# Kernel tuning notes

Measured on AMD Instinct MI355X. Metric: run time of the kernel, lower is better.

Reference implementation:

```python
import jax, jax.numpy as jnp
import numpy as np

EMBED_DIM = 1024
N_HEADS = 16
HEAD_DIM = EMBED_DIM // N_HEADS


def setup_inputs() -> dict:
    key = jax.random.key(0)
    k_x, k_wi, k_bi, k_wo, k_bo = jax.random.split(key, 5)
    B, N, C = 4, 2048, EMBED_DIM
    scale = 1.0 / np.sqrt(C)
    return {
        "x": jax.random.normal(k_x, (B, N, C), dtype=jnp.float32),
        "w_in": jax.random.normal(k_wi, (C, 3 * C), dtype=jnp.float32) * scale,
        "b_in": jax.random.normal(k_bi, (3 * C,), dtype=jnp.float32) * 0.01,
        "w_out": jax.random.normal(k_wo, (C, C), dtype=jnp.float32) * scale,
        "b_out": jax.random.normal(k_bo, (C,), dtype=jnp.float32) * 0.01,
    }


def reference(x, w_in, b_in, w_out, b_out):
    B, N, C = x.shape
    H, D = N_HEADS, HEAD_DIM
    qkv = x @ w_in + b_in  # (B, N, 3C)
    q, k, v = jnp.split(qkv, 3, axis=-1)
    # (B, H, N, D)
    q = q.reshape(B, N, H, D).transpose(0, 2, 1, 3)
    k = k.reshape(B, N, H, D).transpose(0, 2, 1, 3)
    v = v.reshape(B, N, H, D).transpose(0, 2, 1, 3)
    # Naive attention: full (B,H,N,N) scores, NO sqrt(d) scaling (as in source)
    scores = jnp.einsum("bhnd,bhmd->bhnm", q, k)
    attn = jax.nn.softmax(scores, axis=-1)
    out = jnp.einsum("bhnm,bhmd->bhnd", attn, v)
    out = out.transpose(0, 2, 1, 3).reshape(B, N, C)
    return out @ w_out + b_out
```

## Files before the change

### kernel.cpp

```cpp
#include <hip/hip_runtime.h>
#include <hip/hip_bf16.h>
#include <stdint.h>

typedef __attribute__((ext_vector_type(8))) __bf16 bf8v;
typedef __attribute__((ext_vector_type(4))) float f4v;

#define L2E 1.44269504088896f

__device__ __forceinline__ unsigned short f2bf(float f) {
  union { float f; unsigned u; } v; v.f = f;
  unsigned r = v.u + 0x7fffu + ((v.u >> 16) & 1u);
  return (unsigned short)(r >> 16);
}

__device__ __forceinline__ unsigned pk2bf(float f0, float f1) {
  union { __hip_bfloat162 h; unsigned u; } c;
  c.h = __float22bfloat162_rn(make_float2(f0, f1));
  return c.u;
}

__device__ __forceinline__ float exp2_hw(float x) {
  return __builtin_amdgcn_exp2f(x);
}

__device__ __forceinline__ void gl_lds16(const void* g, void* l) {
  __builtin_amdgcn_global_load_lds(
      (__attribute__((address_space(1))) void*)(g),
      (__attribute__((address_space(3))) void*)(l), 16, 0, 0);
}

__global__ void prep_kernel(const float* __restrict__ x,
                            const float* __restrict__ w_in,
                            const float* __restrict__ w_out,
                            unsigned short* __restrict__ xb,
                            unsigned short* __restrict__ wiT,
                            unsigned short* __restrict__ woT) {
  __shared__ float tile[32][33];
  int bx = blockIdx.x;
  if (bx < 8192) {
    int i = bx * 256 + threadIdx.x;
    float4 v = ((const float4*)x)[i];
    ushort4 o;
    o.x = f2bf(v.x); o.y = f2bf(v.y); o.z = f2bf(v.z); o.w = f2bf(v.w);
    ((ushort4*)xb)[i] = o;
    return;
  }
  int idx = bx - 8192;
  int bxx = idx & 127, byy = idx >> 7;
  const float* in; unsigned short* out; int C, c0;
  if (bxx < 96) { in = w_in;  out = wiT; C = 3072; c0 = bxx * 32; }
  else          { in = w_out; out = woT; C = 1024; c0 = (bxx - 96) * 32; }
  int r0 = byy * 32;
  int tx = threadIdx.x & 31, ty = threadIdx.x >> 5;
#pragma unroll
  for (int j = 0; j < 4; ++j)
    tile[ty + 8 * j][tx] = in[(size_t)(r0 + ty + 8 * j) * C + c0 + tx];
  __syncthreads();
#pragma unroll
  for (int j = 0; j < 4; ++j)
    out[(size_t)(c0 + ty + 8 * j) * 1024 + r0 + tx] = f2bf(tile[tx][ty + 8 * j]);
}

template <int MODE>
__global__ __launch_bounds__(512, 2) void gemm256(
    const unsigned short* __restrict__ A,
    const unsigned short* __restrict__ BT,
    const float* __restrict__ bias,
    void* __restrict__ Cv,
    unsigned short* __restrict__ vtg,
    int N, int K, int nbx, float scale) {
  __shared__ __align__(16) unsigned short As[2][256 * 64];
  __shared__ __align__(16) unsigned short Bs[2][128 * 64];
  const int tid = threadIdx.x;
  const int wave = tid >> 6, lane = tid & 63;
  const int lo = lane & 15, hi = lane >> 4;
  const int wm = wave >> 1, wn = wave & 1;

  const int cpx = gridDim.x >> 3;
  const int s = (blockIdx.x & 7) * cpx + (blockIdx.x >> 3);
  const int by = s / nbx, bx = s - by * nbx;
  const int m0 = by * 256, n0 = bx * 128;

  const int srow = lane >> 3;
  const int scol = (((lane & 7) ^ (srow & 7)) * 8);
  const unsigned short* gA = A + (size_t)(m0 + wave * 8 + srow) * K + scol;
  const unsigned short* gB = BT + (size_t)(n0 + wave * 8 + srow) * K + scol;

  const int csw0 = ((hi ^ (lo & 7)) * 8);
  const int csw1 = (((4 + hi) ^ (lo & 7)) * 8);
  const int rA = wm * 64;
  const int rB = wn * 64;

  f4v acc[4][4] = {};
  const int nt = K >> 6;

#pragma unroll
  for (int j = 0; j < 4; ++j)
    gl_lds16(gA + (size_t)(j * 64) * K, &As[0][(j * 64 + wave * 8) * 64]);
#pragma unroll
  for (int j = 0; j < 2; ++j)
    gl_lds16(gB + (size_t)(j * 64) * K, &Bs[0][(j * 64 + wave * 8) * 64]);

  for (int t = 0; t < nt; ++t) {
    const int c = t & 1;
    __builtin_amdgcn_s_barrier();
    __builtin_amdgcn_sched_barrier(0);
    if (t + 1 < nt) {
      const unsigned short* gA1 = gA + (size_t)(t + 1) * 64;
      const unsigned short* gB1 = gB + (size_t)(t + 1) * 64;
#pragma unroll
      for (int j = 0; j < 4; ++j)
        gl_lds16(gA1 + (size_t)(j * 64) * K, &As[c ^ 1][(j * 64 + wave * 8) * 64]);
#pragma unroll
      for (int j = 0; j < 2; ++j)
        gl_lds16(gB1 + (size_t)(j * 64) * K, &Bs[c ^ 1][(j * 64 + wave * 8) * 64]);
      asm volatile("s_waitcnt vmcnt(6)" ::: "memory");
    } else {
      asm volatile("s_waitcnt vmcnt(0)" ::: "memory");
    }
    __builtin_amdgcn_sched_barrier(0);
    __builtin_amdgcn_s_barrier();
    __builtin_amdgcn_sched_barrier(0);

    bf8v b[4][2];
#pragma unroll
    for (int fn = 0; fn < 4; ++fn) {
      b[fn][0] = *(const bf8v*)&Bs[c][(rB + fn * 16 + lo) * 64 + csw0];
      b[fn][1] = *(const bf8v*)&Bs[c][(rB + fn * 16 + lo) * 64 + csw1];
    }
#pragma unroll
    for (int p = 0; p < 2; ++p) {
      bf8v a[2][2];
#pragma unroll
      for (int i = 0; i < 2; ++i) {
        a[i][0] = *(const bf8v*)&As[c][(rA + (p * 2 + i) * 16 + lo) * 64 + csw0];
        a[i][1] = *(const bf8v*)&As[c][(rA + (p * 2 + i) * 16 + lo) * 64 + csw1];
      }
      __builtin_amdgcn_s_setprio(1);
#pragma unroll
      for (int ks = 0; ks < 2; ++ks)
#pragma unroll
        for (int i = 0; i < 2; ++i)
#pragma unroll
          for (int fn = 0; fn < 4; ++fn)
            acc[p * 2 + i][fn] = __builtin_amdgcn_mfma_f32_16x16x32_bf16(
                a[i][ks], b[fn][ks], acc[p * 2 + i][fn], 0, 0, 0);
      __builtin_amdgcn_s_setprio(0);
    }
  }

#pragma unroll
  for (int i = 0; i < 4; ++i) {
#pragma unroll
    for (int j = 0; j < 4; ++j) {
      const int col = n0 + wn * 64 + j * 16 + lo;
      const int row0 = m0 + wm * 64 + i * 16 + hi * 4;
      if (MODE == 0) {
        float* C = (float*)Cv;
#pragma unroll
        for (int r = 0; r < 4; ++r)
          C[(size_t)(row0 + r) * N + col] = acc[i][j][r] + bias[col];
      } else {
        unsigned short* C = (unsigned short*)Cv;
        const float bb = bias[col];
        if (col < 2048) {
          const float sc = (col < 1024) ? scale : 1.0f;
#pragma unroll
          for (int r = 0; r < 4; ++r)
            C[(size_t)(row0 + r) * 2048 + col] = f2bf((acc[i][j][r] + bb) * sc);
        } else {
          const int d = (col - 2048) & 63, hh = (col - 2048) >> 6;
          const int bbt = row0 >> 11, tok = row0 & 2047;
          ushort4 o;
          o.x = f2bf(acc[i][j][0] + bb);
          o.y = f2bf(acc[i][j][1] + bb);
          o.z = f2bf(acc[i][j][2] + bb);
          o.w = f2bf(acc[i][j][3] + bb);
          *(ushort4*)&vtg[((((size_t)bbt * 16 + hh) * 64 + d) * 2048) + tok] = o;
        }
      }
    }
  }
}

#define FSTR 72

__global__ __launch_bounds__(256, 2) void flash_attn(
    const unsigned short* __restrict__ qk,
    const unsigned short* __restrict__ vtg,
    unsigned short* __restrict__ y) {
  __shared__ __align__(16) unsigned short Ps[256 * FSTR];
  __shared__ __align__(16) unsigned short Kt[2][64 * FSTR];
  __shared__ __align__(16) unsigned short Vt[2][64 * FSTR];
  const int tid = threadIdx.x;
  const int wave = tid >> 6, lane = tid & 63;
  const int lo = lane & 15, hi = lane >> 4;

  const int lin = blockIdx.x;
  const int swz = (lin & 7) * 64 + (lin >> 3);
  const int q0 = (swz & 7) << 8;
  const int h  = (swz >> 3) & 15;
  const int b  = swz >> 7;

  const size_t base = (size_t)b * 2048 * 2048;
  const int qoff = h * 64, koff = 1024 + h * 64;
  const unsigned short* vsrc = vtg + (size_t)(b * 16 + h) * 64 * 2048;

  const int m_st = tid >> 3, c_st = tid & 7;
  const unsigned short* kg = qk + base + koff;
  float4 rk0, rk1, rv0, rv1;
  auto kv_load = [&](int kt) {
    const int mb = kt * 64;
    rk0 = *(const float4*)(kg + (size_t)(mb + m_st) * 2048 + c_st * 8);
    rk1 = *(const float4*)(kg + (size_t)(mb + m_st + 32) * 2048 + c_st * 8);
    rv0 = *(const float4*)(vsrc + (size_t)m_st * 2048 + mb + c_st * 8);
    rv1 = *(const float4*)(vsrc + (size_t)(m_st + 32) * 2048 + mb + c_st * 8);
  };
  auto kv_write = [&](int buf) {
    *(float4*)&Kt[buf][m_st * FSTR + c_st * 8] = rk0;
    *(float4*)&Kt[buf][(m_st + 32) * FSTR + c_st * 8] = rk1;
    *(float4*)&Vt[buf][m_st * FSTR + c_st * 8] = rv0;
    *(float4*)&Vt[buf][(m_st + 32) * FSTR + c_st * 8] = rv1;
  };

  kv_load(0);

#pragma unroll
  for (int i = 0; i < 8; ++i) {
    int cid = i * 256 + tid;
    int m = cid >> 3, c = cid & 7;
    *(float4*)&Ps[m * FSTR + c * 8] =
        *(const float4*)(qk + base + (size_t)(q0 + m) * 2048 + qoff + c * 8);
  }
  __syncthreads();
  bf8v bq[4][2];
#pragma unroll
  for (int qt = 0; qt < 4; ++qt)
#pragma unroll
    for (int ks = 0; ks < 2; ++ks)
      bq[qt][ks] = *(const bf8v*)&Ps[(wave * 64 + qt * 16 + lo) * FSTR + ks * 32 + hi * 8];

  f4v O[4][4] = {};
  f4v acc_l[4] = {};
  union { bf8v v; unsigned short u[8]; } onesu;
#pragma unroll
  for (int i = 0; i < 8; ++i) onesu.u[i] = 0x3F80;
  const bf8v ones = onesu.v;

  kv_write(0);
  kv_load(1);
  asm volatile("s_waitcnt lgkmcnt(0)" ::: "memory");
  __builtin_amdgcn_s_barrier();
  asm volatile("" ::: "memory");

  for (int kt = 0; kt < 32; ++kt) {
    const int c = kt & 1;
    if (kt < 31) {
      kv_write(c ^ 1);
      if (kt < 30) kv_load(kt + 2);
    }

#pragma unroll
    for (int ct = 0; ct < 4; ++ct) {
      f4v s[4] = {{}, {}, {}, {}};
      __builtin_amdgcn_s_setprio(1);
#pragma unroll
      for (int ks = 0; ks < 2; ++ks) {
        bf8v ak = *(const bf8v*)&Kt[c][(ct * 16 + lo) * FSTR + ks * 32 + hi * 8];
#pragma unroll
        for (int qt = 0; qt < 4; ++qt)
          s[qt] = __builtin_amdgcn_mfma_f32_16x16x32_bf16(ak, bq[qt][ks], s[qt], 0, 0, 0);
      }
      __builtin_amdgcn_s_setprio(0);
#pragma unroll
      for (int qt = 0; qt < 4; ++qt) {
        float p0 = exp2_hw(s[qt][0]), p1 = exp2_hw(s[qt][1]);
        float p2 = exp2_hw(s[qt][2]), p3 = exp2_hw(s[qt][3]);
        uint2 w; w.x = pk2bf(p0, p1); w.y = pk2bf(p2, p3);
        *(uint2*)&Ps[(wave * 64 + qt * 16 + lo) * FSTR + ct * 16 + hi * 4] = w;
      }
    }

#pragma unroll
    for (int ks = 0; ks < 2; ++ks) {
      bf8v ap[4];
#pragma unroll
      for (int qt = 0; qt < 4; ++qt)
        ap[qt] = *(const bf8v*)&Ps[(wave * 64 + qt * 16 + lo) * FSTR + ks * 32 + hi * 8];
      __builtin_amdgcn_s_setprio(1);
#pragma unroll
      for (int qt = 0; qt < 4; ++qt)
        acc_l[qt] = __builtin_amdgcn_mfma_f32_16x16x32_bf16(ap[qt], ones, acc_l[qt], 0, 0, 0);
#pragma unroll
      for (int dt = 0; dt < 4; ++dt) {
        bf8v bv = *(const bf8v*)&Vt[c][(dt * 16 + lo) * FSTR + ks * 32 + hi * 8];
#pragma unroll
        for (int qt = 0; qt < 4; ++qt)
          O[qt][dt] = __builtin_amdgcn_mfma_f32_16x16x32_bf16(ap[qt], bv, O[qt][dt], 0, 0, 0);
      }
      __builtin_amdgcn_s_setprio(0);
    }

    asm volatile("s_waitcnt lgkmcnt(0)" ::: "memory");
    __builtin_amdgcn_s_barrier();
    asm volatile("" ::: "memory");
  }

#pragma unroll
  for (int qt = 0; qt < 4; ++qt) {
#pragma unroll
    for (int r = 0; r < 4; ++r) {
      float inv = 1.f / acc_l[qt][r];
      int row = q0 + wave * 64 + qt * 16 + hi * 4 + r;
      size_t orow = ((size_t)b * 2048 + row) * 1024 + h * 64;
#pragma unroll
      for (int dt = 0; dt < 4; ++dt)
        y[orow + dt * 16 + lo] = f2bf(O[qt][dt][r] * inv);
    }
  }
}

extern "C" void kernel_launch(void* const* d_in, const int* in_sizes, int n_in,
                              void* d_out, int out_size, void* d_ws, size_t ws_size,
                              hipStream_t stream) {
  (void)in_sizes; (void)n_in; (void)out_size; (void)ws_size;
  const float* x     = (const float*)d_in[0];
  const float* w_in  = (const float*)d_in[1];
  const float* b_in  = (const float*)d_in[2];
  const float* w_out = (const float*)d_in[3];
  const float* b_out = (const float*)d_in[4];

  unsigned short* xb  = (unsigned short*)d_ws;
  unsigned short* wiT = xb  + (size_t)8192 * 1024;
  unsigned short* woT = wiT + (size_t)3072 * 1024;
  unsigned short* qk  = woT + (size_t)1024 * 1024;
  unsigned short* vtg = qk  + (size_t)8192 * 2048;
  unsigned short* yb  = vtg + (size_t)64 * 64 * 2048;

  prep_kernel<<<12288, 256, 0, stream>>>(x, w_in, w_out, xb, wiT, woT);

  gemm256<1><<<768, 512, 0, stream>>>(xb, wiT, b_in, qk, vtg, 3072, 1024, 24, L2E);
  flash_attn<<<512, 256, 0, stream>>>(qk, vtg, yb);
  gemm256<0><<<256, 512, 0, stream>>>(yb, woT, b_out, d_out, nullptr, 1024, 1024, 8, 1.0f);
}
```

Measured before the change: 274.8 us.

## Use 256x256 tiles with eight-phase pipelined staging for QKV projection GEMM

```diff
diff --git a/kernel.cpp b/kernel.cpp
--- a/kernel.cpp
+++ b/kernel.cpp
@@ -61,14 +61,133 @@
     out[(size_t)(c0 + ty + 8 * j) * 1024 + r0 + tx] = f2bf(tile[tx][ty + 8 * j]);
 }
 
-template <int MODE>
-__global__ __launch_bounds__(512, 2) void gemm256(
+__global__ __launch_bounds__(512, 2) void gemm1_8ph(
     const unsigned short* __restrict__ A,
     const unsigned short* __restrict__ BT,
     const float* __restrict__ bias,
-    void* __restrict__ Cv,
+    unsigned short* __restrict__ qk,
     unsigned short* __restrict__ vtg,
-    int N, int K, int nbx, float scale) {
+    int K, int nbx, float scale) {
+  __shared__ __align__(16) unsigned short As[2][256 * 64];
+  __shared__ __align__(16) unsigned short Bs[2][256 * 64];
+  const int tid = threadIdx.x;
+  const int wave = tid >> 6, lane = tid & 63;
+  const int lo = lane & 15, hi = lane >> 4;
+  const int wm = wave >> 2, wn = wave & 3;
+
+  const int cpx = gridDim.x >> 3;
+  const int s = (blockIdx.x & 7) * cpx + (blockIdx.x >> 3);
+  const int by = s / nbx, bx = s - by * nbx;
+  const int m0 = by * 256, n0 = bx * 256;
+
+  const int srow = lane >> 3;
+  const int scol = (((lane & 7) ^ (srow & 7)) * 8);
+  const unsigned short* gA = A + (size_t)(m0 + wave * 8 + srow) * K + scol;
+  const unsigned short* gB = BT + (size_t)(n0 + wave * 8 + srow) * K + scol;
+
+  const int csw0 = ((hi ^ (lo & 7)) * 8);
+  const int csw1 = (((4 + hi) ^ (lo & 7)) * 8);
+  const int rA = wm * 128;
+  const int rB = wn * 64;
+
+  f4v acc[8][4] = {};
+  const int nt = K >> 6;
+
+  auto stageA = [&](int t, int buf, int half) {
+    const unsigned short* g = gA + (size_t)(half * 128) * K + t * 64;
+#pragma unroll
+    for (int j = 0; j < 2; ++j)
+      gl_lds16(g + (size_t)(j * 64) * K, &As[buf][(half * 128 + j * 64 + wave * 8) * 64]);
+  };
+  auto stageB = [&](int t, int buf, int half) {
+    const unsigned short* g = gB + (size_t)(half * 128) * K + t * 64;
+#pragma unroll
+    for (int j = 0; j < 2; ++j)
+      gl_lds16(g + (size_t)(j * 64) * K, &Bs[buf][(half * 128 + j * 64 + wave * 8) * 64]);
+  };
+
+  stageA(0, 0, 0); stageA(0, 0, 1);
+  stageB(0, 0, 0); stageB(0, 0, 1);
+  if (nt > 1) { stageB(1, 1, 0); stageB(1, 1, 1); }
+  asm volatile("s_waitcnt vmcnt(4)" ::: "memory");
+  __builtin_amdgcn_sched_barrier(0);
+  __builtin_amdgcn_s_barrier();
+
+  for (int t = 0; t < nt; ++t) {
+    const int c = t & 1;
+    bf8v b[4][2];
+#pragma unroll
+    for (int p = 0; p < 4; ++p) {
+      if (p == 0) {
+#pragma unroll
+        for (int fn = 0; fn < 4; ++fn) {
+          b[fn][0] = *(const bf8v*)&Bs[c][(rB + fn * 16 + lo) * 64 + csw0];
+          b[fn][1] = *(const bf8v*)&Bs[c][(rB + fn * 16 + lo) * 64 + csw1];
+        }
+      }
+      bf8v a[2][2];
+#pragma unroll
+      for (int i = 0; i < 2; ++i) {
+        a[i][0] = *(const bf8v*)&As[c][(rA + (p * 2 + i) * 16 + lo) * 64 + csw0];
+        a[i][1] = *(const bf8v*)&As[c][(rA + (p * 2 + i) * 16 + lo) * 64 + csw1];
+      }
+      if (p < 2) {
+        if (t + 1 < nt) stageA(t + 1, c ^ 1, p);
+      } else {
+        if (t + 2 < nt) stageB(t + 2, c, p - 2);
+      }
+      if (p == 3 && t + 1 < nt) {
+        if (t + 2 < nt) asm volatile("s_waitcnt vmcnt(4)" ::: "memory");
+        else            asm volatile("s_waitcnt vmcnt(0)" ::: "memory");
+        __builtin_amdgcn_sched_barrier(0);
+      }
+      __builtin_amdgcn_s_barrier();
+      __builtin_amdgcn_s_setprio(1);
+#pragma unroll
+      for (int ks = 0; ks < 2; ++ks)
+#pragma unroll
+        for (int i = 0; i < 2; ++i)
+#pragma unroll
+          for (int fn = 0; fn < 4; ++fn)
+            acc[p * 2 + i][fn] = __builtin_amdgcn_mfma_f32_16x16x32_bf16(
+                a[i][ks], b[fn][ks], acc[p * 2 + i][fn], 0, 0, 0);
+      __builtin_amdgcn_s_setprio(0);
+      __builtin_amdgcn_s_barrier();
+    }
+  }
+
+#pragma unroll
+  for (int i = 0; i < 8; ++i) {
+#pragma unroll
+    for (int j = 0; j < 4; ++j) {
+      const int col = n0 + wn * 64 + j * 16 + lo;
+      const int row0 = m0 + wm * 128 + i * 16 + hi * 4;
+      const float bb = bias[col];
+      if (col < 2048) {
+        const float sc = (col < 1024) ? scale : 1.0f;
+#pragma unroll
+        for (int r = 0; r < 4; ++r)
+          qk[(size_t)(row0 + r) * 2048 + col] = f2bf((acc[i][j][r] + bb) * sc);
+      } else {
+        const int d = (col - 2048) & 63, hh = (col - 2048) >> 6;
+        const int bbt = row0 >> 11, tok = row0 & 2047;
+        ushort4 o;
+        o.x = f2bf(acc[i][j][0] + bb);
+        o.y = f2bf(acc[i][j][1] + bb);
+        o.z = f2bf(acc[i][j][2] + bb);
+        o.w = f2bf(acc[i][j][3] + bb);
+        *(ushort4*)&vtg[((((size_t)bbt * 16 + hh) * 64 + d) * 2048) + tok] = o;
+      }
+    }
+  }
+}
+
+__global__ __launch_bounds__(512, 2) void gemm2k(
+    const unsigned short* __restrict__ A,
+    const unsigned short* __restrict__ BT,
+    const float* __restrict__ bias,
+    float* __restrict__ C,
+    int N, int K, int nbx) {
   __shared__ __align__(16) unsigned short As[2][256 * 64];
   __shared__ __align__(16) unsigned short Bs[2][128 * 64];
   const int tid = threadIdx.x;
@@ -152,32 +271,12 @@
 #pragma unroll
   for (int i = 0; i < 4; ++i) {
 #pragma unroll
-    for (int j = 0; j < 4; ++j) {
-      const int col = n0 + wn * 64 + j * 16 + lo;
-      const int row0 = m0 + wm * 64 + i * 16 + hi * 4;
-      if (MODE == 0) {
-        float* C = (float*)Cv;
-#pragma unroll
-        for (int r = 0; r < 4; ++r)
-          C[(size_t)(row0 + r) * N + col] = acc[i][j][r] + bias[col];
-      } else {
-        unsigned short* C = (unsigned short*)Cv;
-        const float bb = bias[col];
-        if (col < 2048) {
-          const float sc = (col < 1024) ? scale : 1.0f;
-#pragma unroll
-          for (int r = 0; r < 4; ++r)
-            C[(size_t)(row0 + r) * 2048 + col] = f2bf((acc[i][j][r] + bb) * sc);
-        } else {
-          const int d = (col - 2048) & 63, hh = (col - 2048) >> 6;
-          const int bbt = row0 >> 11, tok = row0 & 2047;
-          ushort4 o;
-          o.x = f2bf(acc[i][j][0] + bb);
-          o.y = f2bf(acc[i][j][1] + bb);
-          o.z = f2bf(acc[i][j][2] + bb);
-          o.w = f2bf(acc[i][j][3] + bb);
-          *(ushort4*)&vtg[((((size_t)bbt * 16 + hh) * 64 + d) * 2048) + tok] = o;
-        }
+    for (int r = 0; r < 4; ++r) {
+      int row = m0 + wm * 64 + i * 16 + hi * 4 + r;
+#pragma unroll
+      for (int j = 0; j < 4; ++j) {
+        int col = n0 + wn * 64 + j * 16 + lo;
+        C[(size_t)row * N + col] = acc[i][j][r] + bias[col];
       }
     }
   }
@@ -339,7 +438,7 @@
 
   prep_kernel<<<12288, 256, 0, stream>>>(x, w_in, w_out, xb, wiT, woT);
 
-  gemm256<1><<<768, 512, 0, stream>>>(xb, wiT, b_in, qk, vtg, 3072, 1024, 24, L2E);
+  gemm1_8ph<<<384, 512, 0, stream>>>(xb, wiT, b_in, qk, vtg, 1024, 12, L2E);
   flash_attn<<<512, 256, 0, stream>>>(qk, vtg, yb);
-  gemm256<0><<<256, 512, 0, stream>>>(yb, woT, b_out, d_out, nullptr, 1024, 1024, 8, 1.0f);
-}
+  gemm2k<<<256, 512, 0, stream>>>(yb, woT, b_out, (float*)d_out, 1024, 1024, 8);
+}
```

Result: no change. 272.8 us (-0.7%).
